# Performance work log

Hardware: AMD Instinct MI355X
Metric: run time of the kernel (lower is better)

The kernel has to match this reference:

```python
import jax, jax.numpy as jnp
import numpy as np

B, S, HID, LAYERS, HEADS, WINDOW = 2, 4096, 768, 4, 12, 256
W = WINDOW // 2            # one-sided window: each token attends to W left, W right
HD = HID // HEADS          # head dim = 64
MAXPOS = (S // WINDOW + 1) * WINDOW + 1
EPS = 1e-12                # Longformer layer_norm_eps


def layer_norm(x, g, b):
    m = x.mean(-1, keepdims=True)
    v = ((x - m) ** 2).mean(-1, keepdims=True)
    return (x - m) * jax.lax.rsqrt(v + EPS) * g + b


def sliding_window_attention(q, k, v, key_mask):
    # q,k,v: [B,H,S,D]; key_mask: [B,S] bool. Band attention: |i-j| <= W.
    Bz, Hh, Sl, D = q.shape
    nC = Sl // W
    q = q / jnp.sqrt(jnp.asarray(D, q.dtype))
    cidx = jnp.arange(nC)[:, None] + jnp.arange(3)[None, :]            # [nC,3] chunk gather
    kp = jnp.pad(k, ((0, 0), (0, 0), (W, W), (0, 0))).reshape(Bz, Hh, nC + 2, W, D)
    vp = jnp.pad(v, ((0, 0), (0, 0), (W, W), (0, 0))).reshape(Bz, Hh, nC + 2, W, D)
    kw = kp[:, :, cidx].reshape(Bz, Hh, nC, 3 * W, D)                  # keys for each query chunk
    vw = vp[:, :, cidx].reshape(Bz, Hh, nC, 3 * W, D)
    qc = q.reshape(Bz, Hh, nC, W, D)
    scores = jnp.einsum('bhcqd,bhckd->bhcqk', qc, kw)                  # [B,H,nC,W,3W]
    p = jnp.arange(W)[:, None]
    j = jnp.arange(3 * W)[None, :]
    band = (j >= p) & (j <= p + 2 * W)                                  # [W,3W] banded validity
    keypos = jnp.arange(nC)[:, None, None] * W + j[None] - W           # [nC,1,3W] global key idx
    inrange = (keypos >= 0) & (keypos < Sl)
    kmw = jnp.pad(key_mask, ((0, 0), (W, W))).reshape(Bz, nC + 2, W)[:, cidx].reshape(Bz, nC, 3 * W)
    mask = (band[None] & inrange)[None, None] & kmw[:, None, :, None, :]
    scores = jnp.where(mask, scores, jnp.asarray(-1e9, scores.dtype))
    probs = jax.nn.softmax(scores, axis=-1)
    out = jnp.einsum('bhcqk,bhckd->bhcqd', probs, vw)
    return out.reshape(Bz, Hh, Sl, D)


def heads_split(x):
    return x.reshape(x.shape[0], x.shape[1], HEADS, HD).transpose(0, 2, 1, 3)


def heads_merge(x):
    return x.transpose(0, 2, 1, 3).reshape(x.shape[0], x.shape[2], HID)


def forward(embeddings, pos_emb, tok_emb, emb_ln_g, emb_ln_b, Wq, bq, Wk, bk, Wv, bv,
            Wo, bo, ln1_g, ln1_b, Wi, bi, Wf, bf, ln2_g, ln2_b, Wp, bp, attention_mask):
    Sl = embeddings.shape[1]
    # Longformer embeddings: inputs_embeds + absolute positions (padding_idx+1 .. ) + token type 0
    h = embeddings + pos_emb[1:Sl + 1][None] + tok_emb[0][None, None]
    h = layer_norm(h, emb_ln_g, emb_ln_b)
    km = attention_mask.astype(bool)
    for l in range(LAYERS):
        q = heads_split(h @ Wq[l] + bq[l])
        k = heads_split(h @ Wk[l] + bk[l])
        v = heads_split(h @ Wv[l] + bv[l])
        a = heads_merge(sliding_window_attention(q, k, v, km))
        h = layer_norm(h + (a @ Wo[l] + bo[l]), ln1_g[l], ln1_b[l])
        f = jax.nn.gelu(h @ Wi[l] + bi[l], approximate=False) @ Wf[l] + bf[l]
        h = layer_norm(h + f, ln2_g[l], ln2_b[l])
    return jax.nn.sigmoid((h @ Wp + bp).squeeze(-1))


def setup_inputs() -> dict:
    key = jax.random.key(0)
    ks = jax.random.split(key, 12)
    nrm = lambda k, sh: jax.random.normal(k, sh, jnp.float32) * 0.02
    return dict(
        embeddings=jax.random.normal(ks[0], (B, S, HID), jnp.float32),
        attention_mask=jnp.ones((B, S), jnp.int32),
        pos_emb=nrm(ks[1], (MAXPOS, HID)),
        tok_emb=nrm(ks[2], (2, HID)),
        emb_ln_g=jnp.ones((HID,), jnp.float32),
        emb_ln_b=jnp.zeros((HID,), jnp.float32),
        Wq=nrm(ks[3], (LAYERS, HID, HID)), bq=jnp.zeros((LAYERS, HID), jnp.float32),
        Wk=nrm(ks[4], (LAYERS, HID, HID)), bk=jnp.zeros((LAYERS, HID), jnp.float32),
        Wv=nrm(ks[5], (LAYERS, HID, HID)), bv=jnp.zeros((LAYERS, HID), jnp.float32),
        Wo=nrm(ks[6], (LAYERS, HID, HID)), bo=jnp.zeros((LAYERS, HID), jnp.float32),
        ln1_g=jnp.ones((LAYERS, HID), jnp.float32), ln1_b=jnp.zeros((LAYERS, HID), jnp.float32),
        Wi=nrm(ks[7], (LAYERS, HID, 4 * HID)), bi=jnp.zeros((LAYERS, 4 * HID), jnp.float32),
        Wf=nrm(ks[8], (LAYERS, 4 * HID, HID)), bf=jnp.zeros((LAYERS, HID), jnp.float32),
        ln2_g=jnp.ones((LAYERS, HID), jnp.float32), ln2_b=jnp.zeros((LAYERS, HID), jnp.float32),
        Wp=nrm(ks[9], (HID, 1)), bp=jnp.zeros((1,), jnp.float32),
    )


def reference(embeddings, attention_mask, pos_emb, tok_emb, emb_ln_g, emb_ln_b, Wq, bq, Wk, bk,
              Wv, bv, Wo, bo, ln1_g, ln1_b, Wi, bi, Wf, bf, ln2_g, ln2_b, Wp, bp):
    return forward(embeddings, pos_emb, tok_emb, emb_ln_g, emb_ln_b, Wq, bq, Wk, bk, Wv, bv,
                   Wo, bo, ln1_g, ln1_b, Wi, bi, Wf, bf, ln2_g, ln2_b, Wp, bp, attention_mask)
```

## Files before the change

### kernel.cpp

```cpp
#include <hip/hip_runtime.h>
#include <hip/hip_bf16.h>


typedef __bf16 bf16;
typedef bf16  bf16x8  __attribute__((ext_vector_type(8)));
typedef float floatx4 __attribute__((ext_vector_type(4)));

#define MFMA16(a, b, c) __builtin_amdgcn_mfma_f32_16x16x32_bf16((a), (b), (c), 0, 0, 0)

__device__ __forceinline__ void gld_lds16(const bf16* gp, bf16* lp) {
  __builtin_amdgcn_global_load_lds(
      (const __attribute__((address_space(1))) void*)gp,
      (__attribute__((address_space(3))) void*)lp, 16, 0, 0);
}

__device__ __forceinline__ float fast_rcp(float x) {
  return __builtin_amdgcn_rcpf(x);
}

__device__ __forceinline__ float gelu_fast(float v) {
  float x2 = v * v;
  float u = __builtin_fmaf(x2, -0.07135481f, -1.59576912f);
  float e = __expf(v * u);
  return v * fast_rcp(1.f + e);
}

static constexpr size_t SZ_WTQKV = (size_t)4 * 2304 * 768 * 2;
static constexpr size_t SZ_WTO   = (size_t)4 * 768 * 768 * 2;
static constexpr size_t SZ_WTI   = (size_t)4 * 3072 * 768 * 2;
static constexpr size_t SZ_WTF   = (size_t)4 * 768 * 3072 * 2;
static constexpr size_t SZ_BQKV  = (size_t)4 * 2304 * 4;
static constexpr size_t SZ_H32   = (size_t)8192 * 768 * 4;
static constexpr size_t SZ_HBF   = (size_t)8192 * 768 * 2;
static constexpr size_t SZ_QKV   = (size_t)8192 * 2304 * 2;
static constexpr size_t SZ_ATTN  = (size_t)8192 * 768 * 2;
static constexpr size_t SZ_TMP   = (size_t)8192 * 768 * 4;

static constexpr size_t OFF_WTQKV = 0;
static constexpr size_t OFF_WTO   = OFF_WTQKV + SZ_WTQKV;
static constexpr size_t OFF_WTI   = OFF_WTO   + SZ_WTO;
static constexpr size_t OFF_WTF   = OFF_WTI   + SZ_WTI;
static constexpr size_t OFF_BQKV  = OFF_WTF   + SZ_WTF;
static constexpr size_t OFF_H32   = OFF_BQKV  + SZ_BQKV;
static constexpr size_t OFF_HBF   = OFF_H32   + SZ_H32;
static constexpr size_t OFF_QKV   = OFF_HBF   + SZ_HBF;
static constexpr size_t OFF_ATTN  = OFF_QKV   + SZ_QKV;
static constexpr size_t OFF_TMP   = OFF_ATTN  + SZ_ATTN;
static constexpr size_t OFF_FFN1  = OFF_TMP   + SZ_TMP;

__global__ __launch_bounds__(256) void transpose_cast(
    const float* __restrict__ src, bf16* __restrict__ dst,
    int K, int N, long sStride, long dStride) {
  __shared__ float tile[32][33];
  const int l = blockIdx.z;
  src += (long)l * sStride;
  dst += (long)l * dStride;
  const int n0 = blockIdx.x * 32, k0 = blockIdx.y * 32;
  const int tx = threadIdx.x, ty = threadIdx.y;
#pragma unroll
  for (int i = 0; i < 4; ++i)
    tile[ty + i * 8][tx] = src[(long)(k0 + ty + i * 8) * N + n0 + tx];
  __syncthreads();
#pragma unroll
  for (int i = 0; i < 4; ++i)
    dst[(long)(n0 + ty + i * 8) * K + k0 + tx] = (bf16)tile[tx][ty + i * 8];
}

__global__ void bias_concat(const float* __restrict__ bq, const float* __restrict__ bk,
                            const float* __restrict__ bv, float* __restrict__ bqkv) {
  int i = blockIdx.x * 256 + threadIdx.x;
  if (i >= 4 * 2304) return;
  int l = i / 2304, p = i % 2304;
  float v = (p < 768) ? bq[l * 768 + p]
          : (p < 1536) ? bk[l * 768 + p - 768] : bv[l * 768 + p - 1536];
  bqkv[i] = v;
}

__device__ __forceinline__ void block_stats(float s1, float s2, float* red,
                                            float& mean, float& inv) {
  const int lane = threadIdx.x & 63, wave = threadIdx.x >> 6;
#pragma unroll
  for (int off = 32; off > 0; off >>= 1) {
    s1 += __shfl_down(s1, off, 64);
    s2 += __shfl_down(s2, off, 64);
  }
  if (lane == 0) { red[wave] = s1; red[4 + wave] = s2; }
  __syncthreads();
  s1 = red[0] + red[1] + red[2] + red[3];
  s2 = red[4] + red[5] + red[6] + red[7];
  mean = s1 * (1.f / 768.f);
  float var = s2 * (1.f / 768.f) - mean * mean;
  inv = rsqrtf(var + 1e-12f);
}

__global__ __launch_bounds__(256) void embed_ln_kernel(
    const float* __restrict__ emb, const float* __restrict__ pos,
    const float* __restrict__ tok, const float* __restrict__ g,
    const float* __restrict__ bta, float* __restrict__ h32, bf16* __restrict__ hbf) {
  __shared__ float red[8];
  const long base = (long)blockIdx.x * 768;
  const int s = blockIdx.x & 4095;
  const int t = threadIdx.x;
  float x[3], s1 = 0.f, s2 = 0.f;
#pragma unroll
  for (int i = 0; i < 3; ++i) {
    int c = t + i * 256;
    float v = emb[base + c] + pos[(long)(s + 1) * 768 + c] + tok[c];
    x[i] = v; s1 += v; s2 += v * v;
  }
  float mean, inv;
  block_stats(s1, s2, red, mean, inv);
#pragma unroll
  for (int i = 0; i < 3; ++i) {
    int c = t + i * 256;
    float y = (x[i] - mean) * inv * g[c] + bta[c];
    h32[base + c] = y;
    hbf[base + c] = (bf16)y;
  }
}

__global__ __launch_bounds__(256) void add_ln_kernel(
    float* __restrict__ h32, const bf16* __restrict__ p0,
    const bf16* __restrict__ p1, const float* __restrict__ bias,
    const float* __restrict__ g, const float* __restrict__ bta,
    bf16* __restrict__ hbf) {
  __shared__ float red[8];
  const long base = (long)blockIdx.x * 768;
  const int t = threadIdx.x;
  float x[3], s1 = 0.f, s2 = 0.f;
#pragma unroll
  for (int i = 0; i < 3; ++i) {
    int c = t + i * 256;
    float v = h32[base + c] + (float)p0[base + c] + (float)p1[base + c] + bias[c];
    x[i] = v; s1 += v; s2 += v * v;
  }
  float mean, inv;
  block_stats(s1, s2, red, mean, inv);
#pragma unroll
  for (int i = 0; i < 3; ++i) {
    int c = t + i * 256;
    float y = (x[i] - mean) * inv * g[c] + bta[c];
    h32[base + c] = y;
    hbf[base + c] = (bf16)y;
  }
}

template <int MODE, int N, int LD>
__global__ __launch_bounds__(512, 4) void gemm_kernel(
    const bf16* __restrict__ A, const bf16* __restrict__ BT,
    const float* __restrict__ bias, void* __restrict__ C0, void* __restrict__ C1,
    int ksize) {
  __shared__ bf16 smem[16384];
  bf16* As = smem;
  bf16* Bs = smem + 8192;
  const int tid  = threadIdx.x;
  const int wave = tid >> 6, lane = tid & 63, l15 = lane & 15, quad = lane >> 4;
  const int wm = wave >> 2, wn = wave & 3;
  const long m0 = (long)blockIdx.x * 128;
  const int  n0 = blockIdx.y * 128;
  const int  k0 = blockIdx.z * ksize;

  floatx4 acc[4][2] = {};
  const int rowoff = tid >> 3;
  const int sc_sw = (tid & 7) ^ (rowoff & 7);
  const int fsw = l15 & 7;
  const bf16* Ag = A + m0 * LD + k0 + sc_sw * 8;
  const bf16* Bg = BT + (long)n0 * LD + k0 + sc_sw * 8;

  for (int kt = 0; kt < ksize; kt += 64) {
#pragma unroll
    for (int p = 0; p < 2; ++p) {
      const int row = p * 64 + rowoff;
      gld_lds16(Ag + (long)row * LD + kt, As + p * 4096 + wave * 512);
      gld_lds16(Bg + (long)row * LD + kt, Bs + p * 4096 + wave * 512);
    }
    __syncthreads();
#pragma unroll
    for (int kk = 0; kk < 2; ++kk) {
      const int ch = ((kk * 4 + quad) ^ fsw) * 8;
      bf16x8 af[4], bfr[2];
#pragma unroll
      for (int nt = 0; nt < 2; ++nt)
        bfr[nt] = *(const bf16x8*)&Bs[(wn * 32 + nt * 16 + l15) * 64 + ch];
#pragma unroll
      for (int mt = 0; mt < 4; ++mt)
        af[mt] = *(const bf16x8*)&As[(wm * 64 + mt * 16 + l15) * 64 + ch];
#pragma unroll
      for (int mt = 0; mt < 4; ++mt)
#pragma unroll
        for (int nt = 0; nt < 2; ++nt)
          acc[mt][nt] = MFMA16(af[mt], bfr[nt], acc[mt][nt]);
    }
    __syncthreads();
  }

  bf16* Cg = (bf16*)((MODE == 0 && blockIdx.z != 0) ? C1 : C0);
#pragma unroll
  for (int h = 0; h < 2; ++h) {
    if (wm == h) {
#pragma unroll
      for (int mt = 0; mt < 4; ++mt)
#pragma unroll
        for (int nt = 0; nt < 2; ++nt) {
          const float bb = (MODE == 0) ? 0.f : bias[n0 + wn * 32 + nt * 16 + l15];
#pragma unroll
          for (int r = 0; r < 4; ++r) {
            float v = acc[mt][nt][r] + bb;
            if (MODE == 2) v = gelu_fast(v);
            smem[(mt * 16 + quad * 4 + r) * 136 + wn * 32 + nt * 16 + l15] = (bf16)v;
          }
        }
    }
    __syncthreads();
    {
      const int row = tid >> 3;
#pragma unroll
      for (int p = 0; p < 2; ++p) {
        const int chunk = (tid & 7) + p * 8;
        bf16x8 vv = *(const bf16x8*)&smem[row * 136 + chunk * 8];
        *(bf16x8*)&Cg[(m0 + h * 64 + row) * N + n0 + chunk * 8] = vv;
      }
    }
    __syncthreads();
  }
}

__global__ __launch_bounds__(256) void vtrans_kernel(
    const bf16* __restrict__ qkv, bf16* __restrict__ vt) {
  __shared__ bf16 tile[64 * 68];
  const int s0 = blockIdx.x * 64, h = blockIdx.y, b = blockIdx.z;
  const int tid = threadIdx.x;
  const bf16* src = qkv + (long)b * 4096 * 2304 + 1536 + h * 64;
#pragma unroll
  for (int p = 0; p < 2; ++p) {
    const int i = p * 256 + tid;
    const int r = i >> 3, c = i & 7;
    *(uint4*)&tile[r * 68 + c * 8] = *(const uint4*)&src[(long)(s0 + r) * 2304 + c * 8];
  }
  __syncthreads();
  bf16* dst = vt + ((long)(b * 12 + h)) * 64 * 4096;
#pragma unroll
  for (int p = 0; p < 2; ++p) {
    const int i = p * 256 + tid;
    const int d = i >> 3, cs = i & 7;
    bf16 vals[8];
#pragma unroll
    for (int u = 0; u < 8; ++u) vals[u] = tile[(cs * 8 + u) * 68 + d];
    *(uint4*)&dst[(long)d * 4096 + s0 + cs * 8] = *(const uint4*)vals;
  }
}

__global__ __launch_bounds__(256) void attn_kernel(
    const bf16* __restrict__ qkv, const bf16* __restrict__ vt,
    const int* __restrict__ amask, bf16* __restrict__ attn_out) {
  constexpr int S = 4096, HID3 = 2304;
  __shared__ bf16 Ss[64 * 328];
  __shared__ bf16 Ts[64 * 64];
  __shared__ float redm[64], reds[64];

  const int x = blockIdx.x, q0 = x * 64, h = blockIdx.y, b = blockIdx.z;
  const int tid = threadIdx.x, wave = tid >> 6, lane = tid & 63;
  const int l15 = lane & 15, quad = lane >> 4;
  const int rowoff = tid >> 3;
  const int sc_sw = (tid & 7) ^ (rowoff & 7);
  const int fsw = l15 & 7;
  const int t_lo = (x < 2) ? (2 - x) : 0;
  const int t_hi = (x > 61) ? (66 - x) : 5;

  const bf16* Qb = qkv + (long)b * S * HID3 + h * 64;
  const bf16* Kb = Qb + 768;
  const bf16* Vt_bh = vt + ((long)(b * 12 + h)) * 64 * 4096;

  bf16x8 qf[2];
  {
    const long qrow = q0 + wave * 16 + l15;
    qf[0] = *(const bf16x8*)&Qb[qrow * HID3 + quad * 8];
    qf[1] = *(const bf16x8*)&Qb[qrow * HID3 + 32 + quad * 8];
  }

  float mrow[4] = {-3e38f, -3e38f, -3e38f, -3e38f};

  for (int t = t_lo; t < t_hi; ++t) {
    const int j0 = (x - 2 + t) * 64;
    __syncthreads();
#pragma unroll
    for (int p = 0; p < 2; ++p) {
      const int key = p * 32 + rowoff;
      gld_lds16(Kb + (long)(j0 + key) * HID3 + sc_sw * 8, &Ts[p * 2048 + wave * 512]);
    }
    __syncthreads();
    floatx4 sacc[4] = {};
#pragma unroll
    for (int kk = 0; kk < 2; ++kk) {
      const int ch = ((kk * 4 + quad) ^ fsw) * 8;
#pragma unroll
      for (int nt = 0; nt < 4; ++nt) {
        bf16x8 kf = *(const bf16x8*)&Ts[(nt * 16 + l15) * 64 + ch];
        sacc[nt] = MFMA16(qf[kk], kf, sacc[nt]);
      }
    }
#pragma unroll
    for (int nt = 0; nt < 4; ++nt) {
      const int jj = t * 64 + nt * 16 + l15;
      const int j = j0 + nt * 16 + l15;
      const bool jv = (amask[b * S + j] != 0);
#pragma unroll
      for (int r = 0; r < 4; ++r) {
        const int qi = wave * 16 + quad * 4 + r;
        const bool ok = jv && (jj >= qi) && (jj <= qi + 256);
        const float sv = ok ? sacc[nt][r] * 0.125f : -1e9f;
        mrow[r] = fmaxf(mrow[r], sv);
        Ss[(wave * 16 + quad * 4 + r) * 328 + jj] = (bf16)sv;
      }
    }
  }
#pragma unroll
  for (int off = 1; off < 16; off <<= 1)
#pragma unroll
    for (int r = 0; r < 4; ++r)
      mrow[r] = fmaxf(mrow[r], __shfl_xor(mrow[r], off, 64));
  if (l15 == 0) {
#pragma unroll
    for (int r = 0; r < 4; ++r) redm[wave * 16 + quad * 4 + r] = mrow[r];
  }
  __syncthreads();

  {
    const int row = wave * 16 + l15;
    const float mx = redm[row];
    float sum = 0.f;
    for (int c = t_lo * 8 + quad; c < t_hi * 8; c += 4) {
      bf16x8 pv = *(const bf16x8*)&Ss[row * 328 + c * 8];
#pragma unroll
      for (int u = 0; u < 8; ++u) {
        const float p = __expf((float)pv[u] - mx);
        sum += p;
        pv[u] = (bf16)p;
      }
      *(bf16x8*)&Ss[row * 328 + c * 8] = pv;
    }
    sum += __shfl_xor(sum, 16, 64);
    sum += __shfl_xor(sum, 32, 64);
    if (quad == 0) reds[row] = sum;
  }
  __syncthreads();

  floatx4 oacc[4] = {};
  for (int t = t_lo; t < t_hi; ++t) {
    const int j0 = (x - 2 + t) * 64;
    __syncthreads();
#pragma unroll
    for (int p = 0; p < 2; ++p) {
      const int d = p * 32 + rowoff;
      gld_lds16(Vt_bh + (long)d * 4096 + j0 + sc_sw * 8, &Ts[p * 2048 + wave * 512]);
    }
    __syncthreads();
#pragma unroll
    for (int kk = 0; kk < 2; ++kk) {
      const int ko = kk * 32 + quad * 8;
      const int ch = ((kk * 4 + quad) ^ fsw) * 8;
      bf16x8 pf = *(const bf16x8*)&Ss[(wave * 16 + l15) * 328 + t * 64 + ko];
#pragma unroll
      for (int nt = 0; nt < 4; ++nt) {
        bf16x8 vf = *(const bf16x8*)&Ts[(nt * 16 + l15) * 64 + ch];
        oacc[nt] = MFMA16(pf, vf, oacc[nt]);
      }
    }
  }

  float inv[4];
#pragma unroll
  for (int r = 0; r < 4; ++r) inv[r] = fast_rcp(reds[wave * 16 + quad * 4 + r]);
  const long orow = (long)b * S + q0 + wave * 16 + quad * 4;
#pragma unroll
  for (int nt = 0; nt < 4; ++nt)
#pragma unroll
    for (int r = 0; r < 4; ++r)
      attn_out[(orow + r) * 768 + h * 64 + nt * 16 + l15] =
          (bf16)(oacc[nt][r] * inv[r]);
}

__global__ __launch_bounds__(256) void final_kernel(
    const float* __restrict__ h32, const float* __restrict__ Wp,
    const float* __restrict__ bp, float* __restrict__ out) {
  const int wave = threadIdx.x >> 6, lane = threadIdx.x & 63;
  const long tok = (long)blockIdx.x * 4 + wave;
  float s = 0.f;
#pragma unroll
  for (int i = 0; i < 12; ++i) {
    const int c = lane + i * 64;
    s += h32[tok * 768 + c] * Wp[c];
  }
#pragma unroll
  for (int off = 32; off > 0; off >>= 1) s += __shfl_down(s, off, 64);
  if (lane == 0) out[tok] = fast_rcp(1.f + __expf(-(s + bp[0])));
}

extern "C" void kernel_launch(void* const* d_in, const int* in_sizes, int n_in,
                              void* d_out, int out_size, void* d_ws, size_t ws_size,
                              hipStream_t stream) {
  const float* emb   = (const float*)d_in[0];
  const int*   amask = (const int*)d_in[1];
  const float* pos   = (const float*)d_in[2];
  const float* tok   = (const float*)d_in[3];
  const float* elng  = (const float*)d_in[4];
  const float* elnb  = (const float*)d_in[5];
  const float* Wq = (const float*)d_in[6];   const float* bq = (const float*)d_in[7];
  const float* Wk = (const float*)d_in[8];   const float* bk = (const float*)d_in[9];
  const float* Wv = (const float*)d_in[10];  const float* bv = (const float*)d_in[11];
  const float* Wo = (const float*)d_in[12];  const float* bo = (const float*)d_in[13];
  const float* ln1g = (const float*)d_in[14]; const float* ln1b = (const float*)d_in[15];
  const float* Wi = (const float*)d_in[16];  const float* bi = (const float*)d_in[17];
  const float* Wf = (const float*)d_in[18];  const float* bfb = (const float*)d_in[19];
  const float* ln2g = (const float*)d_in[20]; const float* ln2b = (const float*)d_in[21];
  const float* Wp = (const float*)d_in[22];  const float* bp = (const float*)d_in[23];
  float* out = (float*)d_out;

  char* ws = (char*)d_ws;
  bf16*  WTqkv = (bf16*)(ws + OFF_WTQKV);
  bf16*  WTo   = (bf16*)(ws + OFF_WTO);
  bf16*  WTi   = (bf16*)(ws + OFF_WTI);
  bf16*  WTf   = (bf16*)(ws + OFF_WTF);
  float* bqkv  = (float*)(ws + OFF_BQKV);
  float* h32   = (float*)(ws + OFF_H32);
  bf16*  hbf   = (bf16*)(ws + OFF_HBF);
  bf16*  qkvb  = (bf16*)(ws + OFF_QKV);
  bf16*  part1 = (bf16*)(ws + OFF_QKV);
  bf16*  attnb = (bf16*)(ws + OFF_ATTN);
  bf16*  part0 = (bf16*)(ws + OFF_TMP);
  bf16*  vtb   = (bf16*)(ws + OFF_TMP);
  bf16*  ffn1  = (bf16*)(ws + OFF_FFN1);

  const dim3 tb(32, 8, 1);
  transpose_cast<<<dim3(24, 24, 4), tb, 0, stream>>>(Wq, WTqkv,               768, 768,  (long)768 * 768,  (long)2304 * 768);
  transpose_cast<<<dim3(24, 24, 4), tb, 0, stream>>>(Wk, WTqkv + 768 * 768,   768, 768,  (long)768 * 768,  (long)2304 * 768);
  transpose_cast<<<dim3(24, 24, 4), tb, 0, stream>>>(Wv, WTqkv + 1536 * 768,  768, 768,  (long)768 * 768,  (long)2304 * 768);
  transpose_cast<<<dim3(24, 24, 4), tb, 0, stream>>>(Wo, WTo,                 768, 768,  (long)768 * 768,  (long)768 * 768);
  transpose_cast<<<dim3(96, 24, 4), tb, 0, stream>>>(Wi, WTi,                 768, 3072, (long)768 * 3072, (long)3072 * 768);
  transpose_cast<<<dim3(24, 96, 4), tb, 0, stream>>>(Wf, WTf,                 3072, 768, (long)3072 * 768, (long)768 * 3072);
  bias_concat<<<36, 256, 0, stream>>>(bq, bk, bv, bqkv);

  embed_ln_kernel<<<8192, 256, 0, stream>>>(emb, pos, tok, elng, elnb, h32, hbf);

  for (int l = 0; l < 4; ++l) {
    gemm_kernel<1, 2304, 768><<<dim3(64, 18, 1), 512, 0, stream>>>(
        hbf, WTqkv + (size_t)l * 2304 * 768, bqkv + l * 2304, qkvb, nullptr, 768);
    vtrans_kernel<<<dim3(64, 12, 2), 256, 0, stream>>>(qkvb, vtb);
    attn_kernel<<<dim3(64, 12, 2), 256, 0, stream>>>(qkvb, vtb, amask, attnb);
    gemm_kernel<0, 768, 768><<<dim3(64, 6, 2), 512, 0, stream>>>(
        attnb, WTo + (size_t)l * 768 * 768, nullptr, part0, part1, 384);
    add_ln_kernel<<<8192, 256, 0, stream>>>(h32, part0, part1, bo + l * 768,
                                            ln1g + l * 768, ln1b + l * 768, hbf);
    gemm_kernel<2, 3072, 768><<<dim3(64, 24, 1), 512, 0, stream>>>(
        hbf, WTi + (size_t)l * 3072 * 768, bi + l * 3072, ffn1, nullptr, 768);
    gemm_kernel<0, 768, 3072><<<dim3(64, 6, 2), 512, 0, stream>>>(
        ffn1, WTf + (size_t)l * 768 * 3072, nullptr, part0, part1, 1536);
    add_ln_kernel<<<8192, 256, 0, stream>>>(h32, part0, part1, bfb + l * 768,
                                            ln2g + l * 768, ln2b + l * 768, hbf);
  }

  final_kernel<<<2048, 256, 0, stream>>>(h32, Wp, bp, out);
}
```

Baseline: 1.146 ms.

## Double-buffer GEMM LDS tiles to overlap global loads with MFMA

```diff
diff --git a/kernel.cpp b/kernel.cpp
--- a/kernel.cpp
+++ b/kernel.cpp
@@ -7,6 +7,10 @@
 typedef float floatx4 __attribute__((ext_vector_type(4)));
 
 #define MFMA16(a, b, c) __builtin_amdgcn_mfma_f32_16x16x32_bf16((a), (b), (c), 0, 0, 0)
+
+#define BARR() __builtin_amdgcn_s_barrier()
+#define VMC4() asm volatile("s_waitcnt vmcnt(4)" ::: "memory")
+#define VMC0() asm volatile("s_waitcnt vmcnt(0)" ::: "memory")
 
 __device__ __forceinline__ void gld_lds16(const bf16* gp, bf16* lp) {
   __builtin_amdgcn_global_load_lds(
@@ -150,9 +154,7 @@
     const bf16* __restrict__ A, const bf16* __restrict__ BT,
     const float* __restrict__ bias, void* __restrict__ C0, void* __restrict__ C1,
     int ksize) {
-  __shared__ bf16 smem[16384];
-  bf16* As = smem;
-  bf16* Bs = smem + 8192;
+  __shared__ bf16 smem[32768];
   const int tid  = threadIdx.x;
   const int wave = tid >> 6, lane = tid & 63, l15 = lane & 15, quad = lane >> 4;
   const int wm = wave >> 2, wn = wave & 3;
@@ -166,15 +168,33 @@
   const int fsw = l15 & 7;
   const bf16* Ag = A + m0 * LD + k0 + sc_sw * 8;
   const bf16* Bg = BT + (long)n0 * LD + k0 + sc_sw * 8;
-
-  for (int kt = 0; kt < ksize; kt += 64) {
-#pragma unroll
-    for (int p = 0; p < 2; ++p) {
-      const int row = p * 64 + rowoff;
-      gld_lds16(Ag + (long)row * LD + kt, As + p * 4096 + wave * 512);
-      gld_lds16(Bg + (long)row * LD + kt, Bs + p * 4096 + wave * 512);
-    }
-    __syncthreads();
+  const int nk = ksize >> 6;
+
+#pragma unroll
+  for (int p = 0; p < 2; ++p) {
+    const int row = p * 64 + rowoff;
+    gld_lds16(Ag + (long)row * LD, smem + p * 4096 + wave * 512);
+    gld_lds16(Bg + (long)row * LD, smem + 8192 + p * 4096 + wave * 512);
+  }
+
+  for (int kt = 0; kt < nk; ++kt) {
+    const int cur = kt & 1;
+    if (kt + 1 < nk) {
+      bf16* nb = smem + (cur ^ 1) * 16384;
+      const int off = (kt + 1) * 64;
+#pragma unroll
+      for (int p = 0; p < 2; ++p) {
+        const int row = p * 64 + rowoff;
+        gld_lds16(Ag + (long)row * LD + off, nb + p * 4096 + wave * 512);
+        gld_lds16(Bg + (long)row * LD + off, nb + 8192 + p * 4096 + wave * 512);
+      }
+      VMC4();
+    } else {
+      VMC0();
+    }
+    BARR();
+    const bf16* As = smem + cur * 16384;
+    const bf16* Bs = As + 8192;
 #pragma unroll
     for (int kk = 0; kk < 2; ++kk) {
       const int ch = ((kk * 4 + quad) ^ fsw) * 8;
@@ -191,7 +211,7 @@
         for (int nt = 0; nt < 2; ++nt)
           acc[mt][nt] = MFMA16(af[mt], bfr[nt], acc[mt][nt]);
     }
-    __syncthreads();
+    BARR();
   }
 
   bf16* Cg = (bf16*)((MODE == 0 && blockIdx.z != 0) ? C1 : C0);
```

After: 1.160 ms. No clear change (+1.2%).
